# Kernel tuning notes

Measured on AMD Instinct MI355X. Metric: run time of the kernel, lower is better.

Reference implementation:

```python
import jax, jax.numpy as jnp
import numpy as np

N = 65536   # total nodes
E = 1048576 # total edges (avg degree 16)
B = 512     # graphs in batch
H = 4       # gat1 heads
C = 64      # per-head channels / GNN_HIDDEN


def segment_softmax(logits, seg, num_segments):
    # numerically stable softmax over segments (PyG softmax semantics, eps=1e-16)
    m = jax.ops.segment_max(logits, seg, num_segments=num_segments)
    m = jnp.where(jnp.isfinite(m), m, 0.0)
    e = jnp.exp(logits - m[seg])
    s = jax.ops.segment_sum(e, seg, num_segments=num_segments)
    return e / (s[seg] + 1e-16)


def gat_conv(x, edge_index, edge_attr, W, att_src, att_dst, We, att_edge, bias, heads, out_ch, concat):
    # PyG GATConv with edge_dim, add_self_loops=False
    n = x.shape[0]
    h = (x @ W).reshape(n, heads, out_ch)                 # (N,H,C)
    src, dst = edge_index[0], edge_index[1]
    a_s = jnp.sum(h * att_src, axis=-1)                   # (N,H)
    a_d = jnp.sum(h * att_dst, axis=-1)                   # (N,H)
    he = (edge_attr @ We).reshape(-1, heads, out_ch)      # (E,H,C)
    a_e = jnp.sum(he * att_edge, axis=-1)                 # (E,H)
    alpha = jax.nn.leaky_relu(a_s[src] + a_d[dst] + a_e, negative_slope=0.2)
    alpha = segment_softmax(alpha, dst, n)                # softmax over incoming edges per dst
    out = jax.ops.segment_sum(h[src] * alpha[..., None], dst, num_segments=n)  # (N,H,C)
    out = out.reshape(n, heads * out_ch) if concat else out.mean(axis=1)
    return out + bias


def setup_inputs() -> dict:
    key = jax.random.key(0)
    ks = jax.random.split(key, 24)
    s = 0.05
    d = {}
    d["global_feat"] = jax.random.normal(ks[0], (B, 512), jnp.float32)
    d["x"] = jax.random.normal(ks[1], (N, 13), jnp.float32)
    d["roi_feats"] = jax.random.normal(ks[2], (N, 256), jnp.float32)
    d["edge_index"] = jax.random.randint(ks[3], (2, E), 0, N)
    d["edge_attr"] = jax.random.normal(ks[4], (E, 5), jnp.float32)
    d["batch_vec"] = jnp.sort(jax.random.randint(ks[5], (N,), 0, B))
    # roi_proj / scene_proj
    d["roi_W"] = jax.random.normal(ks[6], (256, 64), jnp.float32) * s
    d["roi_b"] = jnp.zeros((64,), jnp.float32)
    d["scene_W"] = jax.random.normal(ks[7], (512, 128), jnp.float32) * s
    d["scene_b"] = jnp.zeros((128,), jnp.float32)
    d["g1_W"] = jax.random.normal(ks[8], (77, H * C), jnp.float32) * s
    d["g1_att_src"] = jax.random.normal(ks[9], (H, C), jnp.float32) * s
    d["g1_att_dst"] = jax.random.normal(ks[10], (H, C), jnp.float32) * s
    d["g1_We"] = jax.random.normal(ks[11], (5, H * C), jnp.float32) * s
    d["g1_att_edge"] = jax.random.normal(ks[12], (H, C), jnp.float32) * s
    d["g1_bias"] = jnp.zeros((H * C,), jnp.float32)
    # gat2: 256 -> 64, 1 head
    d["g2_W"] = jax.random.normal(ks[13], (H * C, C), jnp.float32) * s
    d["g2_att_src"] = jax.random.normal(ks[14], (1, C), jnp.float32) * s
    d["g2_att_dst"] = jax.random.normal(ks[15], (1, C), jnp.float32) * s
    d["g2_We"] = jax.random.normal(ks[16], (5, C), jnp.float32) * s
    d["g2_att_edge"] = jax.random.normal(ks[17], (1, C), jnp.float32) * s
    d["g2_bias"] = jnp.zeros((C,), jnp.float32)
    # attention pooling gate + classifier
    d["gate_W"] = jax.random.normal(ks[18], (C, 1), jnp.float32) * s
    d["gate_b"] = jnp.zeros((1,), jnp.float32)
    d["cls1_W"] = jax.random.normal(ks[19], (128 + C, 64), jnp.float32) * s
    d["cls1_b"] = jnp.zeros((64,), jnp.float32)
    d["cls2_W"] = jax.random.normal(ks[20], (64, 3), jnp.float32) * s
    d["cls2_b"] = jnp.zeros((3,), jnp.float32)
    return d


def reference(global_feat, x, roi_feats, edge_index, edge_attr, batch_vec,
              roi_W, roi_b, scene_W, scene_b,
              g1_W, g1_att_src, g1_att_dst, g1_We, g1_att_edge, g1_bias,
              g2_W, g2_att_src, g2_att_dst, g2_We, g2_att_edge, g2_bias,
              gate_W, gate_b, cls1_W, cls1_b, cls2_W, cls2_b):
    scene = global_feat @ scene_W + scene_b                       # (B,128)
    vis = jax.nn.relu(roi_feats @ roi_W + roi_b)                  # (N,64)
    h = jnp.concatenate([x, vis], axis=-1)                        # (N,77)
    h = jax.nn.relu(gat_conv(h, edge_index, edge_attr, g1_W, g1_att_src, g1_att_dst, g1_We, g1_att_edge, g1_bias, H, C, True))
    h = gat_conv(h, edge_index, edge_attr, g2_W, g2_att_src, g2_att_dst, g2_We, g2_att_edge, g2_bias, 1, C, False)  # (N,64)
    # GlobalAttention pooling
    gate = segment_softmax((h @ gate_W + gate_b)[:, 0], batch_vec, B)
    rel = jax.ops.segment_sum(gate[:, None] * h, batch_vec, num_segments=B)  # (B,64)
    comb = jnp.concatenate([scene, rel], axis=-1)                 # (B,192)
    hid = jax.nn.relu(comb @ cls1_W + cls1_b)                     # dropout off (eval)
    return hid @ cls2_W + cls2_b                                  # (B,3)
```

## Files before the change

### kernel.cpp

```cpp
#include <hip/hip_runtime.h>

#define N_NODES 65536
#define N_EDGES 1048576
#define NB      512

typedef unsigned short u16;
typedef unsigned int   u32;
typedef unsigned long long u64;

typedef __attribute__((ext_vector_type(8))) short bf16x8;
typedef __attribute__((ext_vector_type(4))) float f32x4;

__device__ __forceinline__ float bf2f(u16 u) { return __uint_as_float(((u32)u) << 16); }
__device__ __forceinline__ float lo16(u32 u) { return __uint_as_float(u << 16); }
__device__ __forceinline__ float hi16(u32 u) { return __uint_as_float(u & 0xffff0000u); }
__device__ __forceinline__ u16 f2bf(float f) {
    u32 u = __float_as_uint(f);
    u32 r = (u + 0x7fffu + ((u >> 16) & 1u)) >> 16;
    return (u16)r;
}
__device__ __forceinline__ u32 pk2(float a, float b) {
    return (u32)f2bf(a) | ((u32)f2bf(b) << 16);
}
__device__ __forceinline__ float wsum(float v) {
    for (int o = 32; o; o >>= 1) v += __shfl_xor(v, o, 64);
    return v;
}
__device__ __forceinline__ float wmax(float v) {
    for (int o = 32; o; o >>= 1) v = fmaxf(v, __shfl_xor(v, o, 64));
    return v;
}

__global__ void k_prep(const float* g1We, const float* g1ae, const float* g2We, const float* g2ae,
                       float* M1, float* M2) {
    int t = threadIdx.x;
    if (t < 20) {
        int j = t >> 2, h = t & 3;
        float s = 0.f;
        for (int c = 0; c < 64; c++) s += g1We[j * 256 + h * 64 + c] * g1ae[h * 64 + c];
        M1[t] = s;
    } else if (t < 25) {
        int j = t - 20;
        float s = 0.f;
        for (int c = 0; c < 64; c++) s += g2We[j * 64 + c] * g2ae[c];
        M2[j] = s;
    }
}

__global__ void k_wt1(const float* __restrict__ g1W, u16* __restrict__ Wt) {
    int c = blockIdx.x;
    int k = threadIdx.x;
    float v = 0.f;
    if (k < 77) {
        int ko = (k < 64) ? (13 + k) : (k - 64);
        v = g1W[(size_t)ko * 256 + c];
    }
    Wt[(size_t)c * 96 + k] = f2bf(v);
}

__global__ void k_wtv(const float* __restrict__ W, u16* __restrict__ Wt) {
    int c = blockIdx.x;
    int k = threadIdx.x;
    Wt[(size_t)c * 256 + k] = f2bf(W[(size_t)k * 64 + c]);
}

__global__ __launch_bounds__(256) void k_scene(const float* __restrict__ gf, const float* __restrict__ W,
                                               const float* __restrict__ bias, float* __restrict__ scene) {
    int idx = blockIdx.x * 256 + threadIdx.x;
    int b = idx >> 7, j = idx & 127;
    float acc = 0.f;
    for (int k = 0; k < 512; k++) acc += gf[b * 512 + k] * W[k * 128 + j];
    scene[idx] = acc + bias[j];
}

__global__ __launch_bounds__(256) void k_hist(const int* ei, int* cnt) {
    int e = blockIdx.x * 256 + threadIdx.x;
    atomicAdd(&cnt[ei[N_EDGES + e]], 1);
}

__global__ __launch_bounds__(256) void k_scan_blk(const int* __restrict__ cnt, int* __restrict__ pre,
                                                  int* __restrict__ bsum) {
    __shared__ int sd[256];
    int t = threadIdx.x, b = blockIdx.x;
    int base = b * 1024 + t * 4;
    int4 c = *(const int4*)(cnt + base);
    int s = c.x + c.y + c.z + c.w;
    sd[t] = s;
    __syncthreads();
    for (int off = 1; off < 256; off <<= 1) {
        int v = (t >= off) ? sd[t - off] : 0;
        __syncthreads();
        sd[t] += v;
        __syncthreads();
    }
    int excl = sd[t] - s;
    int4 p;
    p.x = excl;
    p.y = excl + c.x;
    p.z = excl + c.x + c.y;
    p.w = excl + c.x + c.y + c.z;
    *(int4*)(pre + base) = p;
    if (t == 255) bsum[b] = sd[255];
}

__global__ __launch_bounds__(64) void k_scan_top(int* bsum) {
    int t = threadIdx.x;
    int v = bsum[t];
    int inc = v;
    for (int off = 1; off < 64; off <<= 1) {
        int u = __shfl_up(inc, off, 64);
        if (t >= off) inc += u;
    }
    bsum[t] = inc - v;
}

__global__ __launch_bounds__(256) void k_scan_fix(const int* __restrict__ pre, const int* __restrict__ bsum,
                                                  int* __restrict__ row_ptr, int* __restrict__ coarse_cur) {
    int i = blockIdx.x * 256 + threadIdx.x;
    int v = pre[i] + bsum[i >> 10];
    row_ptr[i] = v;
    if ((i & 255) == 0) coarse_cur[i >> 8] = v;
    if (i == 0) row_ptr[N_NODES] = N_EDGES;
}

__global__ __launch_bounds__(256) void k_bucket(const int* __restrict__ ei, int* coarse_cur,
                                                u32* __restrict__ bpack, int* __restrict__ bsrc) {
    __shared__ u32 stageP[4096];
    __shared__ int stageS[4096];
    __shared__ int bcnt[256], bscan[256], boff[256], gbase[256];
    int t = threadIdx.x;
    int e0 = blockIdx.x * 4096;
    bcnt[t] = 0;
    __syncthreads();
    int dreg[16], sreg[16];
    for (int it = 0; it < 16; it++) {
        int e = e0 + it * 256 + t;
        int dd = ei[N_EDGES + e];
        dreg[it] = dd;
        sreg[it] = ei[e];
        atomicAdd(&bcnt[dd >> 8], 1);
    }
    __syncthreads();
    int v = bcnt[t];
    bscan[t] = v;
    __syncthreads();
    for (int off = 1; off < 256; off <<= 1) {
        int u = (t >= off) ? bscan[t - off] : 0;
        __syncthreads();
        bscan[t] += u;
        __syncthreads();
    }
    boff[t] = bscan[t] - v;
    gbase[t] = v ? atomicAdd(&coarse_cur[t], v) : 0;
    __syncthreads();
    for (int it = 0; it < 16; it++) {
        int e = e0 + it * 256 + t;
        int b = dreg[it] >> 8;
        int pos = atomicAdd(&boff[b], 1);
        stageP[pos] = ((u32)e << 12) | (u32)(dreg[it] & 255);
        stageS[pos] = sreg[it];
    }
    __syncthreads();
    for (int idx = t; idx < 4096; idx += 256) {
        int lo = 0, hi = 255;
        while (lo < hi) { int mid = (lo + hi) >> 1; if (bscan[mid] > idx) hi = mid; else lo = mid + 1; }
        int b = lo;
        int g = gbase[b] + (idx - (bscan[b] - bcnt[b]));
        bpack[g] = stageP[idx];
        bsrc[g] = stageS[idx];
    }
}

__global__ __launch_bounds__(256) void k_sortb(const u32* __restrict__ bpack, const int* __restrict__ bsrc,
                                               const int* __restrict__ row_ptr,
                                               int* __restrict__ eord, int* __restrict__ ssrc) {
    __shared__ int cur[256];
    int t = threadIdx.x, b = blockIdx.x;
    int nbase = b * 256;
    cur[t] = row_ptr[nbase + t];
    __syncthreads();
    int beg = row_ptr[nbase];
    int end = row_ptr[nbase + 256];
    for (int i = beg + t; i < end; i += 256) {
        u32 wd = bpack[i];
        int src = bsrc[i];
        int d8 = wd & 255;
        int pos = atomicAdd(&cur[d8], 1);
        eord[pos] = (int)(wd >> 12);
        ssrc[pos] = src;
    }
}

__global__ __launch_bounds__(256) void k_payload(const int* __restrict__ eord, const float* __restrict__ ea,
                                                 const float* __restrict__ M1, const float* __restrict__ M2,
                                                 float* __restrict__ a1es, float* __restrict__ a2es) {
    int pos = blockIdx.x * 256 + threadIdx.x;
    int e = eord[pos];
    float v[5];
    for (int j = 0; j < 5; j++) v[j] = ea[(size_t)e * 5 + j];
    float4 o;
    o.x = v[0]*M1[0]  + v[1]*M1[4]  + v[2]*M1[8]  + v[3]*M1[12] + v[4]*M1[16];
    o.y = v[0]*M1[1]  + v[1]*M1[5]  + v[2]*M1[9]  + v[3]*M1[13] + v[4]*M1[17];
    o.z = v[0]*M1[2]  + v[1]*M1[6]  + v[2]*M1[10] + v[3]*M1[14] + v[4]*M1[18];
    o.w = v[0]*M1[3]  + v[1]*M1[7]  + v[2]*M1[11] + v[3]*M1[15] + v[4]*M1[19];
    *(float4*)(a1es + (size_t)pos * 4) = o;
    a2es[pos] = v[0]*M2[0] + v[1]*M2[1] + v[2]*M2[2] + v[3]*M2[3] + v[4]*M2[4];
}

__global__ __launch_bounds__(256) void k_vis(const float* __restrict__ roi, const u16* __restrict__ Wt,
                                             const float* __restrict__ bias, u16* __restrict__ out) {
    __shared__ u16 At[64][264];
    int t = threadIdx.x;
    int w = t >> 6, l = t & 63, lo = l & 15, hi = l >> 4;
    int n0 = blockIdx.x * 64;
    int r = t >> 2, sub = t & 3;
    const float* rp = roi + (size_t)(n0 + r) * 256 + sub * 4;
    #pragma unroll
    for (int q = 0; q < 16; q++) {
        float4 v = *(const float4*)(rp + q * 16);
        uint2 p;
        p.x = pk2(v.x, v.y);
        p.y = pk2(v.z, v.w);
        *(uint2*)&At[r][q * 16 + sub * 4] = p;
    }
    float bb[4][4];
    #pragma unroll
    for (int cb = 0; cb < 4; cb++)
        #pragma unroll
        for (int rg = 0; rg < 4; rg++) bb[cb][rg] = bias[cb * 16 + hi * 4 + rg];
    __syncthreads();
    f32x4 acc[4];
    #pragma unroll
    for (int cb = 0; cb < 4; cb++) acc[cb] = (f32x4){0.f, 0.f, 0.f, 0.f};
    #pragma unroll
    for (int ks = 0; ks < 8; ks++) {
        bf16x8 af = *(const bf16x8*)(&At[w * 16 + lo][ks * 32 + hi * 8]);
        #pragma unroll
        for (int cb = 0; cb < 4; cb++) {
            bf16x8 wf = *(const bf16x8*)(Wt + (size_t)(cb * 16 + lo) * 256 + ks * 32 + hi * 8);
            acc[cb] = __builtin_amdgcn_mfma_f32_16x16x32_bf16(wf, af, acc[cb], 0, 0, 0);
        }
    }
    int nrow = n0 + w * 16 + lo;
    #pragma unroll
    for (int cb = 0; cb < 4; cb++) {
        uint2 p;
        p.x = pk2(fmaxf(acc[cb][0] + bb[cb][0], 0.f), fmaxf(acc[cb][1] + bb[cb][1], 0.f));
        p.y = pk2(fmaxf(acc[cb][2] + bb[cb][2], 0.f), fmaxf(acc[cb][3] + bb[cb][3], 0.f));
        *(uint2*)(out + (size_t)nrow * 64 + cb * 16 + hi * 4) = p;
    }
}

__global__ __launch_bounds__(256) void k_h1(const float* __restrict__ x, const u16* __restrict__ vis,
                                            const u16* __restrict__ Wt,
                                            const float* __restrict__ as_, const float* __restrict__ ad_,
                                            u16* __restrict__ h1, float* __restrict__ a1s,
                                            float* __restrict__ a1d) {
    __shared__ u16 At[64][104];
    int t = threadIdx.x;
    int w = t >> 6, l = t & 63, lo = l & 15, hi = l >> 4;
    int n0 = blockIdx.x * 64;
    int r = t >> 2, sub = t & 3;
    {
        const uint4* vp = (const uint4*)(vis + (size_t)(n0 + r) * 64 + sub * 16);
        uint4 v0 = vp[0], v1 = vp[1];
        *(uint4*)&At[r][sub * 16] = v0;
        *(uint4*)&At[r][sub * 16 + 8] = v1;
        if (sub == 0) {
            const float* xp = x + (size_t)(n0 + r) * 13;
            #pragma unroll
            for (int j = 0; j < 13; j++) At[r][64 + j] = f2bf(xp[j]);
        } else if (sub == 1) {
            #pragma unroll
            for (int j = 77; j < 96; j++) At[r][j] = 0;
        }
    }
    bf16x8 wf[4][3];
    float asv[4][4], adv[4][4];
    #pragma unroll
    for (int cb = 0; cb < 4; cb++) {
        #pragma unroll
        for (int ks = 0; ks < 3; ks++)
            wf[cb][ks] = *(const bf16x8*)(Wt + (size_t)(w * 64 + cb * 16 + lo) * 96 + ks * 32 + hi * 8);
        #pragma unroll
        for (int rg = 0; rg < 4; rg++) {
            asv[cb][rg] = as_[w * 64 + cb * 16 + hi * 4 + rg];
            adv[cb][rg] = ad_[w * 64 + cb * 16 + hi * 4 + rg];
        }
    }
    __syncthreads();
    #pragma unroll
    for (int nb = 0; nb < 4; nb++) {
        f32x4 acc[4];
        #pragma unroll
        for (int cb = 0; cb < 4; cb++) acc[cb] = (f32x4){0.f, 0.f, 0.f, 0.f};
        #pragma unroll
        for (int ks = 0; ks < 3; ks++) {
            bf16x8 af = *(const bf16x8*)(&At[nb * 16 + lo][ks * 32 + hi * 8]);
            #pragma unroll
            for (int cb = 0; cb < 4; cb++)
                acc[cb] = __builtin_amdgcn_mfma_f32_16x16x32_bf16(wf[cb][ks], af, acc[cb], 0, 0, 0);
        }
        int nrow = n0 + nb * 16 + lo;
        float ps = 0.f, pd = 0.f;
        #pragma unroll
        for (int cb = 0; cb < 4; cb++) {
            uint2 p;
            p.x = pk2(acc[cb][0], acc[cb][1]);
            p.y = pk2(acc[cb][2], acc[cb][3]);
            *(uint2*)(h1 + (size_t)nrow * 256 + w * 64 + cb * 16 + hi * 4) = p;
            ps += acc[cb][0] * asv[cb][0] + acc[cb][1] * asv[cb][1]
                + acc[cb][2] * asv[cb][2] + acc[cb][3] * asv[cb][3];
            pd += acc[cb][0] * adv[cb][0] + acc[cb][1] * adv[cb][1]
                + acc[cb][2] * adv[cb][2] + acc[cb][3] * adv[cb][3];
        }
        ps += __shfl_xor(ps, 16, 64); ps += __shfl_xor(ps, 32, 64);
        pd += __shfl_xor(pd, 16, 64); pd += __shfl_xor(pd, 32, 64);
        if (hi == 0) {
            a1s[nrow * 4 + w] = ps;
            a1d[nrow * 4 + w] = pd;
        }
    }
}

__global__ __launch_bounds__(256) void k_h2(const u16* __restrict__ A, const u16* __restrict__ Wt,
                                            const float* __restrict__ as_, const float* __restrict__ ad_,
                                            u16* __restrict__ out, float* __restrict__ a2s,
                                            float* __restrict__ a2d) {
    int t = threadIdx.x;
    int w = t >> 6, l = t & 63, lo = l & 15, hi = l >> 4;
    int nrow = blockIdx.x * 64 + w * 16 + lo;
    f32x4 acc[4];
    #pragma unroll
    for (int cb = 0; cb < 4; cb++) acc[cb] = (f32x4){0.f, 0.f, 0.f, 0.f};
    const u16* ap = A + (size_t)nrow * 256 + hi * 8;
    #pragma unroll
    for (int ks = 0; ks < 8; ks++) {
        bf16x8 af = *(const bf16x8*)(ap + ks * 32);
        #pragma unroll
        for (int cb = 0; cb < 4; cb++) {
            bf16x8 wf = *(const bf16x8*)(Wt + (size_t)(cb * 16 + lo) * 256 + ks * 32 + hi * 8);
            acc[cb] = __builtin_amdgcn_mfma_f32_16x16x32_bf16(wf, af, acc[cb], 0, 0, 0);
        }
    }
    float ps = 0.f, pd = 0.f;
    #pragma unroll
    for (int cb = 0; cb < 4; cb++) {
        uint2 p;
        p.x = pk2(acc[cb][0], acc[cb][1]);
        p.y = pk2(acc[cb][2], acc[cb][3]);
        *(uint2*)(out + (size_t)nrow * 64 + cb * 16 + hi * 4) = p;
        #pragma unroll
        for (int rg = 0; rg < 4; rg++) {
            float a = acc[cb][rg];
            ps += a * as_[cb * 16 + hi * 4 + rg];
            pd += a * ad_[cb * 16 + hi * 4 + rg];
        }
    }
    ps += __shfl_xor(ps, 16, 64); ps += __shfl_xor(ps, 32, 64);
    pd += __shfl_xor(pd, 16, 64); pd += __shfl_xor(pd, 32, 64);
    if (hi == 0) {
        a2s[nrow] = ps;
        a2d[nrow] = pd;
    }
}

__global__ __launch_bounds__(256) void k_sg1(const int* __restrict__ row_ptr, const int* __restrict__ ssrc,
                                             const float* __restrict__ a1s, const float* __restrict__ a1d,
                                             const float* __restrict__ a1es, const u16* __restrict__ h1,
                                             const float* __restrict__ bias, u16* __restrict__ out1) {
    __shared__ float wl[4][1024];
    int t = threadIdx.x;
    int wv = t >> 6, L = t & 63;
    int n = blockIdx.x * 4 + wv;
    int beg = row_ptr[n], deg = row_ptr[n + 1] - beg;
    int lim = (deg < 256) ? deg : 256;
    {
        int h = L >> 4, j = L & 15;
        float adn = a1d[n * 4 + h];
        float m = -3.0e38f, s = 0.f;
        for (int i = j; i < deg; i += 16) {
            int pos = beg + i;
            float l = a1s[ssrc[pos] * 4 + h] + adn + a1es[(size_t)pos * 4 + h];
            l = (l > 0.f) ? l : 0.2f * l;
            if (i < 256) wl[wv][i * 4 + h] = l;
            if (l > m) { s = s * __expf(m - l) + 1.f; m = l; }
            else       { s += __expf(l - m); }
        }
        for (int o = 1; o < 16; o <<= 1) {
            float mo = __shfl_xor(m, o, 64), so = __shfl_xor(s, o, 64);
            float M = fmaxf(m, mo);
            s = s * __expf(m - M) + so * __expf(mo - M);
            m = M;
        }
        float inv = 1.f / (s + 1e-16f);
        for (int i = j; i < lim; i += 16)
            wl[wv][i * 4 + h] = __expf(wl[wv][i * 4 + h] - m) * inv;
    }
    __syncthreads();
    int halfE = L >> 5;
    int L32 = L & 31;
    int hd = L32 >> 3;
    float acc[8];
    #pragma unroll
    for (int j = 0; j < 8; j++) acc[j] = 0.f;
    int last = beg + deg - 1;
    for (int i = 0; i < deg; i += 8) {
        int iA = i + halfE, iB = i + 2 + halfE, iC = i + 4 + halfE, iD = i + 6 + halfE;
        bool vA = iA < deg, vB = iB < deg, vC = iC < deg, vD = iD < deg;
        int cA = vA ? beg + iA : last, cB = vB ? beg + iB : last;
        int cC = vC ? beg + iC : last, cD = vD ? beg + iD : last;
        int sA = ssrc[cA], sB = ssrc[cB], sC = ssrc[cC], sD = ssrc[cD];
        float wA = vA ? wl[wv][iA * 4 + hd] : 0.f;
        float wB = vB ? wl[wv][iB * 4 + hd] : 0.f;
        float wC = vC ? wl[wv][iC * 4 + hd] : 0.f;
        float wD = vD ? wl[wv][iD * 4 + hd] : 0.f;
        uint4 uA = *((const uint4*)(h1 + (size_t)sA * 256) + L32);
        uint4 uB = *((const uint4*)(h1 + (size_t)sB * 256) + L32);
        uint4 uC = *((const uint4*)(h1 + (size_t)sC * 256) + L32);
        uint4 uD = *((const uint4*)(h1 + (size_t)sD * 256) + L32);
        acc[0] += wA * lo16(uA.x) + wB * lo16(uB.x) + wC * lo16(uC.x) + wD * lo16(uD.x);
        acc[1] += wA * hi16(uA.x) + wB * hi16(uB.x) + wC * hi16(uC.x) + wD * hi16(uD.x);
        acc[2] += wA * lo16(uA.y) + wB * lo16(uB.y) + wC * lo16(uC.y) + wD * lo16(uD.y);
        acc[3] += wA * hi16(uA.y) + wB * hi16(uB.y) + wC * hi16(uC.y) + wD * hi16(uD.y);
        acc[4] += wA * lo16(uA.z) + wB * lo16(uB.z) + wC * lo16(uC.z) + wD * lo16(uD.z);
        acc[5] += wA * hi16(uA.z) + wB * hi16(uB.z) + wC * hi16(uC.z) + wD * hi16(uD.z);
        acc[6] += wA * lo16(uA.w) + wB * lo16(uB.w) + wC * lo16(uC.w) + wD * lo16(uD.w);
        acc[7] += wA * hi16(uA.w) + wB * hi16(uB.w) + wC * hi16(uC.w) + wD * hi16(uD.w);
    }
    #pragma unroll
    for (int j = 0; j < 8; j++) acc[j] += __shfl_xor(acc[j], 32, 64);
    if (halfE == 0) {
        float4 b0 = *(const float4*)(bias + 8 * L32);
        float4 b1 = *(const float4*)(bias + 8 * L32 + 4);
        uint4 pk;
        pk.x = (u32)f2bf(fmaxf(acc[0] + b0.x, 0.f)) | ((u32)f2bf(fmaxf(acc[1] + b0.y, 0.f)) << 16);
        pk.y = (u32)f2bf(fmaxf(acc[2] + b0.z, 0.f)) | ((u32)f2bf(fmaxf(acc[3] + b0.w, 0.f)) << 16);
        pk.z = (u32)f2bf(fmaxf(acc[4] + b1.x, 0.f)) | ((u32)f2bf(fmaxf(acc[5] + b1.y, 0.f)) << 16);
        pk.w = (u32)f2bf(fmaxf(acc[6] + b1.z, 0.f)) | ((u32)f2bf(fmaxf(acc[7] + b1.w, 0.f)) << 16);
        *((uint4*)(out1 + (size_t)n * 256) + L32) = pk;
    }
}

__global__ __launch_bounds__(256) void k_sg2(const int* __restrict__ row_ptr, const int* __restrict__ ssrc,
                                             const float* __restrict__ a2s, const float* __restrict__ a2d,
                                             const float* __restrict__ a2es, const u16* __restrict__ h2b,
                                             const float* __restrict__ bias, float* __restrict__ hfin) {
    __shared__ float wl[4][256];
    int t = threadIdx.x;
    int wv = t >> 6, L = t & 63;
    int n = blockIdx.x * 4 + wv;
    int beg = row_ptr[n], deg = row_ptr[n + 1] - beg;
    int lim = (deg < 256) ? deg : 256;
    {
        float adn = a2d[n];
        float m = -3.0e38f, s = 0.f;
        for (int i = L; i < deg; i += 64) {
            int pos = beg + i;
            float l = a2s[ssrc[pos]] + adn + a2es[pos];
            l = (l > 0.f) ? l : 0.2f * l;
            if (i < 256) wl[wv][i] = l;
            if (l > m) { s = s * __expf(m - l) + 1.f; m = l; }
            else       { s += __expf(l - m); }
        }
        for (int o = 1; o < 64; o <<= 1) {
            float mo = __shfl_xor(m, o, 64), so = __shfl_xor(s, o, 64);
            float M = fmaxf(m, mo);
            s = s * __expf(m - M) + so * __expf(mo - M);
            m = M;
        }
        float inv = 1.f / (s + 1e-16f);
        for (int i = L; i < lim; i += 64)
            wl[wv][i] = __expf(wl[wv][i] - m) * inv;
    }
    __syncthreads();
    int halfE = L >> 5;
    int L32 = L & 31;
    float a0 = 0.f, a1v = 0.f;
    int last = beg + deg - 1;
    const u32* h2u = (const u32*)h2b;
    for (int i = 0; i < deg; i += 8) {
        int iA = i + halfE, iB = i + 2 + halfE, iC = i + 4 + halfE, iD = i + 6 + halfE;
        bool vA = iA < deg, vB = iB < deg, vC = iC < deg, vD = iD < deg;
        int cA = vA ? beg + iA : last, cB = vB ? beg + iB : last;
        int cC = vC ? beg + iC : last, cD = vD ? beg + iD : last;
        int sA = ssrc[cA], sB = ssrc[cB], sC = ssrc[cC], sD = ssrc[cD];
        float wA = vA ? wl[wv][iA] : 0.f;
        float wB = vB ? wl[wv][iB] : 0.f;
        float wC = vC ? wl[wv][iC] : 0.f;
        float wD = vD ? wl[wv][iD] : 0.f;
        u32 uA = h2u[(size_t)sA * 32 + L32];
        u32 uB = h2u[(size_t)sB * 32 + L32];
        u32 uC = h2u[(size_t)sC * 32 + L32];
        u32 uD = h2u[(size_t)sD * 32 + L32];
        a0  += wA * lo16(uA) + wB * lo16(uB) + wC * lo16(uC) + wD * lo16(uD);
        a1v += wA * hi16(uA) + wB * hi16(uB) + wC * hi16(uC) + wD * hi16(uD);
    }
    a0  += __shfl_xor(a0, 32, 64);
    a1v += __shfl_xor(a1v, 32, 64);
    if (halfE == 0) {
        float2 o;
        o.x = a0  + bias[2 * L32];
        o.y = a1v + bias[2 * L32 + 1];
        *(float2*)(hfin + (size_t)n * 64 + 2 * L32) = o;
    }
}

__global__ __launch_bounds__(64) void k_pool(const int* __restrict__ bvec, const float* __restrict__ hf,
                                             const float* gateW, const float* gateb,
                                             const float* __restrict__ scene,
                                             const float* c1W, const float* c1b,
                                             const float* c2W, const float* c2b,
                                             float* __restrict__ outp) {
    int b = blockIdx.x, lane = threadIdx.x;
    __shared__ float gwl[64], se[64], comb[192], hid[64];
    gwl[lane] = gateW[lane];
    __syncthreads();
    int s0, s1;
    { int lo = 0, hi = N_NODES; while (lo < hi) { int mid = (lo + hi) >> 1; if (bvec[mid] < b) lo = mid + 1; else hi = mid; } s0 = lo; }
    { int lo = 0, hi = N_NODES; while (lo < hi) { int mid = (lo + hi) >> 1; if (bvec[mid] < b + 1) lo = mid + 1; else hi = mid; } s1 = lo; }
    float gb = gateb[0];
    float m = -3.0e38f, ssum = 0.f, acc = 0.f;
    for (int cs = s0; cs < s1; cs += 64) {
        int cnt = min(64, s1 - cs);
        float l = -3.0e38f;
        if (lane < cnt) {
            int n = cs + lane;
            float d = 0.f;
            for (int i = 0; i < 64; i++) d += hf[(size_t)n * 64 + i] * gwl[i];
            l = d + gb;
        }
        float cm = wmax(l);
        float newm = fmaxf(m, cm);
        float rsc = __expf(m - newm);
        float e = (lane < cnt) ? __expf(l - newm) : 0.f;
        float es = wsum(e);
        ssum = ssum * rsc + es;
        se[lane] = e;
        __syncthreads();
        float a2 = 0.f;
        for (int i = 0; i < cnt; i++) a2 += se[i] * hf[(size_t)(cs + i) * 64 + lane];
        acc = acc * rsc + a2;
        __syncthreads();
        m = newm;
    }
    float rel = acc / (ssum + 1e-16f);
    comb[lane] = scene[b * 128 + lane];
    comb[64 + lane] = scene[b * 128 + 64 + lane];
    comb[128 + lane] = rel;
    __syncthreads();
    float hj = 0.f;
    for (int k = 0; k < 192; k++) hj += comb[k] * c1W[k * 64 + lane];
    hj += c1b[lane];
    hid[lane] = fmaxf(hj, 0.f);
    __syncthreads();
    if (lane < 3) {
        float o = 0.f;
        for (int k = 0; k < 64; k++) o += hid[k] * c2W[k * 3 + lane];
        o += c2b[lane];
        outp[b * 3 + lane] = o;
    }
}

extern "C" void kernel_launch(void* const* d_in, const int* in_sizes, int n_in,
                              void* d_out, int out_size, void* d_ws, size_t ws_size,
                              hipStream_t stream) {
    (void)in_sizes; (void)n_in; (void)out_size; (void)ws_size;
    const float* gf     = (const float*)d_in[0];
    const float* x      = (const float*)d_in[1];
    const float* roi    = (const float*)d_in[2];
    const int*   ei     = (const int*)d_in[3];
    const float* ea     = (const float*)d_in[4];
    const int*   bvec   = (const int*)d_in[5];
    const float* roiW   = (const float*)d_in[6];
    const float* roib   = (const float*)d_in[7];
    const float* sceneW = (const float*)d_in[8];
    const float* sceneb = (const float*)d_in[9];
    const float* g1W    = (const float*)d_in[10];
    const float* g1as   = (const float*)d_in[11];
    const float* g1ad   = (const float*)d_in[12];
    const float* g1We   = (const float*)d_in[13];
    const float* g1ae   = (const float*)d_in[14];
    const float* g1b    = (const float*)d_in[15];
    const float* g2W    = (const float*)d_in[16];
    const float* g2as   = (const float*)d_in[17];
    const float* g2ad   = (const float*)d_in[18];
    const float* g2We   = (const float*)d_in[19];
    const float* g2ae   = (const float*)d_in[20];
    const float* g2b    = (const float*)d_in[21];
    const float* gateW  = (const float*)d_in[22];
    const float* gateb  = (const float*)d_in[23];
    const float* c1W    = (const float*)d_in[24];
    const float* c1b    = (const float*)d_in[25];
    const float* c2W    = (const float*)d_in[26];
    const float* c2b    = (const float*)d_in[27];

    char* w = (char*)d_ws;
    size_t o = 0;
    auto nxt = [&](size_t bytes) -> char* {
        char* p = w + o;
        o += (bytes + 255) & ~(size_t)255;
        return p;
    };
    float* scene  = (float*)nxt((size_t)NB * 128 * 4);
    float* M1     = (float*)nxt(80);
    float* M2     = (float*)nxt(32);
    u16* g1Wt     = (u16*)nxt((size_t)256 * 96 * 2);
    u16* roiWt    = (u16*)nxt((size_t)64 * 256 * 2);
    u16* g2Wt     = (u16*)nxt((size_t)64 * 256 * 2);
    int* cnt      = (int*)nxt((size_t)N_NODES * 4);
    int* pre      = (int*)nxt((size_t)N_NODES * 4);
    int* bsum     = (int*)nxt(64 * 4);
    int* row_ptr  = (int*)nxt((size_t)(N_NODES + 1) * 4);
    int* coarse   = (int*)nxt(256 * 4);
    u32* bpack    = (u32*)nxt((size_t)N_EDGES * 4);
    int* bsrc     = (int*)nxt((size_t)N_EDGES * 4);
    int* eord     = (int*)nxt((size_t)N_EDGES * 4);
    int* ssrc     = (int*)nxt((size_t)N_EDGES * 4);
    float* a1es   = (float*)nxt((size_t)N_EDGES * 16);
    float* a2es   = (float*)nxt((size_t)N_EDGES * 4);
    u16* visb     = (u16*)nxt((size_t)N_NODES * 64 * 2);
    u16* h1       = (u16*)nxt((size_t)N_NODES * 256 * 2);
    u16* out1     = (u16*)nxt((size_t)N_NODES * 256 * 2);
    u16* h2b      = (u16*)nxt((size_t)N_NODES * 64 * 2);
    float* hfin   = (float*)nxt((size_t)N_NODES * 64 * 4);
    float* a1s    = (float*)nxt((size_t)N_NODES * 16);
    float* a1d    = (float*)nxt((size_t)N_NODES * 16);
    float* a2s    = (float*)nxt((size_t)N_NODES * 4);
    float* a2d    = (float*)nxt((size_t)N_NODES * 4);

    hipMemsetAsync(cnt, 0, (size_t)N_NODES * 4, stream);
    k_prep<<<1, 32, 0, stream>>>(g1We, g1ae, g2We, g2ae, M1, M2);
    k_wt1<<<256, 96, 0, stream>>>(g1W, g1Wt);
    k_wtv<<<64, 256, 0, stream>>>(roiW, roiWt);
    k_wtv<<<64, 256, 0, stream>>>(g2W, g2Wt);
    k_scene<<<(NB * 128) / 256, 256, 0, stream>>>(gf, sceneW, sceneb, scene);
    k_hist<<<N_EDGES / 256, 256, 0, stream>>>(ei, cnt);
    k_scan_blk<<<64, 256, 0, stream>>>(cnt, pre, bsum);
    k_scan_top<<<1, 64, 0, stream>>>(bsum);
    k_scan_fix<<<N_NODES / 256, 256, 0, stream>>>(pre, bsum, row_ptr, coarse);
    k_bucket<<<256, 256, 0, stream>>>(ei, coarse, bpack, bsrc);
    k_sortb<<<256, 256, 0, stream>>>(bpack, bsrc, row_ptr, eord, ssrc);
    k_payload<<<N_EDGES / 256, 256, 0, stream>>>(eord, ea, M1, M2, a1es, a2es);
    k_vis<<<N_NODES / 64, 256, 0, stream>>>(roi, roiWt, roib, visb);
    k_h1<<<N_NODES / 64, 256, 0, stream>>>(x, visb, g1Wt, g1as, g1ad, h1, a1s, a1d);
    k_sg1<<<N_NODES / 4, 256, 0, stream>>>(row_ptr, ssrc, a1s, a1d, a1es, h1, g1b, out1);
    k_h2<<<N_NODES / 64, 256, 0, stream>>>(out1, g2Wt, g2as, g2ad, h2b, a2s, a2d);
    k_sg2<<<N_NODES / 4, 256, 0, stream>>>(row_ptr, ssrc, a2s, a2d, a2es, h2b, g2b, hfin);
    k_pool<<<NB, 64, 0, stream>>>(bvec, hfin, gateW, gateb, scene, c1W, c1b, c2W, c2b, (float*)d_out);
}
```

Baseline: 527.4 us.

## Fuse weight prep kernels, fold edge payload into sort, prefetch gathers in aggregation

Merges the four weight-preparation kernels into one launch and folds the edge-attribute payload computation into the bucket-sort kernel, which removes the eord array and one pass over edges. The bucket kernel now takes 2048 edges per block across twice as many blocks. Both aggregation kernels cache source indices in shared memory during the softmax pass and software-prefetch the next group of neighbor rows. The block-wide barrier is replaced with a compiler fence plus s_waitcnt, which relies on each wave only reading its own shared-memory slice. The payload computation now runs per edge inside the sort loop, with scattered edge_attr reads.

New measurement: 538.4 us. 2.1% more time.

```diff
diff --git a/kernel.cpp b/kernel.cpp
--- a/kernel.cpp
+++ b/kernel.cpp
@@ -31,37 +31,44 @@
     return v;
 }
 
-__global__ void k_prep(const float* g1We, const float* g1ae, const float* g2We, const float* g2ae,
-                       float* M1, float* M2) {
-    int t = threadIdx.x;
-    if (t < 20) {
-        int j = t >> 2, h = t & 3;
-        float s = 0.f;
-        for (int c = 0; c < 64; c++) s += g1We[j * 256 + h * 64 + c] * g1ae[h * 64 + c];
-        M1[t] = s;
-    } else if (t < 25) {
-        int j = t - 20;
-        float s = 0.f;
-        for (int c = 0; c < 64; c++) s += g2We[j * 64 + c] * g2ae[c];
-        M2[j] = s;
-    }
-}
-
-__global__ void k_wt1(const float* __restrict__ g1W, u16* __restrict__ Wt) {
-    int c = blockIdx.x;
-    int k = threadIdx.x;
-    float v = 0.f;
-    if (k < 77) {
-        int ko = (k < 64) ? (13 + k) : (k - 64);
-        v = g1W[(size_t)ko * 256 + c];
-    }
-    Wt[(size_t)c * 96 + k] = f2bf(v);
-}
-
-__global__ void k_wtv(const float* __restrict__ W, u16* __restrict__ Wt) {
-    int c = blockIdx.x;
-    int k = threadIdx.x;
-    Wt[(size_t)c * 256 + k] = f2bf(W[(size_t)k * 64 + c]);
+__global__ __launch_bounds__(512) void k_wprep(const float* __restrict__ g1W, const float* __restrict__ roiW,
+                                               const float* __restrict__ g2W,
+                                               const float* __restrict__ g1We, const float* __restrict__ g1ae,
+                                               const float* __restrict__ g2We, const float* __restrict__ g2ae,
+                                               u16* __restrict__ g1Wt, u16* __restrict__ roiWt,
+                                               u16* __restrict__ g2Wt, float* __restrict__ M1,
+                                               float* __restrict__ M2) {
+    int b = blockIdx.x, t = threadIdx.x;
+    if (b < 48) {
+        int idx = b * 512 + t;
+        int c = idx / 96, k = idx - 96 * c;
+        float v = 0.f;
+        if (k < 77) {
+            int ko = (k < 64) ? (13 + k) : (k - 64);
+            v = g1W[(size_t)ko * 256 + c];
+        }
+        g1Wt[idx] = f2bf(v);
+    } else if (b < 80) {
+        int idx = (b - 48) * 512 + t;
+        int c = idx >> 8, k = idx & 255;
+        roiWt[idx] = f2bf(roiW[(size_t)k * 64 + c]);
+    } else if (b < 112) {
+        int idx = (b - 80) * 512 + t;
+        int c = idx >> 8, k = idx & 255;
+        g2Wt[idx] = f2bf(g2W[(size_t)k * 64 + c]);
+    } else {
+        if (t < 20) {
+            int j = t >> 2, h = t & 3;
+            float s = 0.f;
+            for (int c = 0; c < 64; c++) s += g1We[j * 256 + h * 64 + c] * g1ae[h * 64 + c];
+            M1[t] = s;
+        } else if (t < 25) {
+            int j = t - 20;
+            float s = 0.f;
+            for (int c = 0; c < 64; c++) s += g2We[j * 64 + c] * g2ae[c];
+            M2[j] = s;
+        }
+    }
 }
 
 __global__ __launch_bounds__(256) void k_scene(const float* __restrict__ gf, const float* __restrict__ W,
@@ -125,15 +132,15 @@
 
 __global__ __launch_bounds__(256) void k_bucket(const int* __restrict__ ei, int* coarse_cur,
                                                 u32* __restrict__ bpack, int* __restrict__ bsrc) {
-    __shared__ u32 stageP[4096];
-    __shared__ int stageS[4096];
+    __shared__ u32 stageP[2048];
+    __shared__ int stageS[2048];
     __shared__ int bcnt[256], bscan[256], boff[256], gbase[256];
     int t = threadIdx.x;
-    int e0 = blockIdx.x * 4096;
+    int e0 = blockIdx.x * 2048;
     bcnt[t] = 0;
     __syncthreads();
-    int dreg[16], sreg[16];
-    for (int it = 0; it < 16; it++) {
+    int dreg[8], sreg[8];
+    for (int it = 0; it < 8; it++) {
         int e = e0 + it * 256 + t;
         int dd = ei[N_EDGES + e];
         dreg[it] = dd;
@@ -153,7 +160,7 @@
     boff[t] = bscan[t] - v;
     gbase[t] = v ? atomicAdd(&coarse_cur[t], v) : 0;
     __syncthreads();
-    for (int it = 0; it < 16; it++) {
+    for (int it = 0; it < 8; it++) {
         int e = e0 + it * 256 + t;
         int b = dreg[it] >> 8;
         int pos = atomicAdd(&boff[b], 1);
@@ -161,7 +168,7 @@
         stageS[pos] = sreg[it];
     }
     __syncthreads();
-    for (int idx = t; idx < 4096; idx += 256) {
+    for (int idx = t; idx < 2048; idx += 256) {
         int lo = 0, hi = 255;
         while (lo < hi) { int mid = (lo + hi) >> 1; if (bscan[mid] > idx) hi = mid; else lo = mid + 1; }
         int b = lo;
@@ -171,40 +178,40 @@
     }
 }
 
-__global__ __launch_bounds__(256) void k_sortb(const u32* __restrict__ bpack, const int* __restrict__ bsrc,
-                                               const int* __restrict__ row_ptr,
-                                               int* __restrict__ eord, int* __restrict__ ssrc) {
+__global__ __launch_bounds__(256) void k_sortp(const u32* __restrict__ bpack, const int* __restrict__ bsrc,
+                                               const int* __restrict__ row_ptr, const float* __restrict__ ea,
+                                               const float* __restrict__ M1, const float* __restrict__ M2,
+                                               int* __restrict__ ssrc, float* __restrict__ a1es,
+                                               float* __restrict__ a2es) {
     __shared__ int cur[256];
     int t = threadIdx.x, b = blockIdx.x;
     int nbase = b * 256;
     cur[t] = row_ptr[nbase + t];
     __syncthreads();
+    float m1[20], m2[5];
+    #pragma unroll
+    for (int j = 0; j < 20; j++) m1[j] = M1[j];
+    #pragma unroll
+    for (int j = 0; j < 5; j++) m2[j] = M2[j];
     int beg = row_ptr[nbase];
     int end = row_ptr[nbase + 256];
     for (int i = beg + t; i < end; i += 256) {
         u32 wd = bpack[i];
         int src = bsrc[i];
         int d8 = wd & 255;
+        int e = (int)(wd >> 12);
         int pos = atomicAdd(&cur[d8], 1);
-        eord[pos] = (int)(wd >> 12);
         ssrc[pos] = src;
-    }
-}
-
-__global__ __launch_bounds__(256) void k_payload(const int* __restrict__ eord, const float* __restrict__ ea,
-                                                 const float* __restrict__ M1, const float* __restrict__ M2,
-                                                 float* __restrict__ a1es, float* __restrict__ a2es) {
-    int pos = blockIdx.x * 256 + threadIdx.x;
-    int e = eord[pos];
-    float v[5];
-    for (int j = 0; j < 5; j++) v[j] = ea[(size_t)e * 5 + j];
-    float4 o;
-    o.x = v[0]*M1[0]  + v[1]*M1[4]  + v[2]*M1[8]  + v[3]*M1[12] + v[4]*M1[16];
-    o.y = v[0]*M1[1]  + v[1]*M1[5]  + v[2]*M1[9]  + v[3]*M1[13] + v[4]*M1[17];
-    o.z = v[0]*M1[2]  + v[1]*M1[6]  + v[2]*M1[10] + v[3]*M1[14] + v[4]*M1[18];
-    o.w = v[0]*M1[3]  + v[1]*M1[7]  + v[2]*M1[11] + v[3]*M1[15] + v[4]*M1[19];
-    *(float4*)(a1es + (size_t)pos * 4) = o;
-    a2es[pos] = v[0]*M2[0] + v[1]*M2[1] + v[2]*M2[2] + v[3]*M2[3] + v[4]*M2[4];
+        const float* ep = ea + (size_t)e * 5;
+        float v0 = ep[0], v1 = ep[1], v2 = ep[2], v3 = ep[3], v4 = ep[4];
+        float4 o;
+        o.x = v0*m1[0]  + v1*m1[4]  + v2*m1[8]  + v3*m1[12] + v4*m1[16];
+        o.y = v0*m1[1]  + v1*m1[5]  + v2*m1[9]  + v3*m1[13] + v4*m1[17];
+        o.z = v0*m1[2]  + v1*m1[6]  + v2*m1[10] + v3*m1[14] + v4*m1[18];
+        o.w = v0*m1[3]  + v1*m1[7]  + v2*m1[11] + v3*m1[15] + v4*m1[19];
+        *(float4*)(a1es + (size_t)pos * 4) = o;
+        a2es[pos] = v0*m2[0] + v1*m2[1] + v2*m2[2] + v3*m2[3] + v4*m2[4];
+    }
 }
 
 __global__ __launch_bounds__(256) void k_vis(const float* __restrict__ roi, const u16* __restrict__ Wt,
@@ -323,53 +330,12 @@
     }
 }
 
-__global__ __launch_bounds__(256) void k_h2(const u16* __restrict__ A, const u16* __restrict__ Wt,
-                                            const float* __restrict__ as_, const float* __restrict__ ad_,
-                                            u16* __restrict__ out, float* __restrict__ a2s,
-                                            float* __restrict__ a2d) {
-    int t = threadIdx.x;
-    int w = t >> 6, l = t & 63, lo = l & 15, hi = l >> 4;
-    int nrow = blockIdx.x * 64 + w * 16 + lo;
-    f32x4 acc[4];
-    #pragma unroll
-    for (int cb = 0; cb < 4; cb++) acc[cb] = (f32x4){0.f, 0.f, 0.f, 0.f};
-    const u16* ap = A + (size_t)nrow * 256 + hi * 8;
-    #pragma unroll
-    for (int ks = 0; ks < 8; ks++) {
-        bf16x8 af = *(const bf16x8*)(ap + ks * 32);
-        #pragma unroll
-        for (int cb = 0; cb < 4; cb++) {
-            bf16x8 wf = *(const bf16x8*)(Wt + (size_t)(cb * 16 + lo) * 256 + ks * 32 + hi * 8);
-            acc[cb] = __builtin_amdgcn_mfma_f32_16x16x32_bf16(wf, af, acc[cb], 0, 0, 0);
-        }
-    }
-    float ps = 0.f, pd = 0.f;
-    #pragma unroll
-    for (int cb = 0; cb < 4; cb++) {
-        uint2 p;
-        p.x = pk2(acc[cb][0], acc[cb][1]);
-        p.y = pk2(acc[cb][2], acc[cb][3]);
-        *(uint2*)(out + (size_t)nrow * 64 + cb * 16 + hi * 4) = p;
-        #pragma unroll
-        for (int rg = 0; rg < 4; rg++) {
-            float a = acc[cb][rg];
-            ps += a * as_[cb * 16 + hi * 4 + rg];
-            pd += a * ad_[cb * 16 + hi * 4 + rg];
-        }
-    }
-    ps += __shfl_xor(ps, 16, 64); ps += __shfl_xor(ps, 32, 64);
-    pd += __shfl_xor(pd, 16, 64); pd += __shfl_xor(pd, 32, 64);
-    if (hi == 0) {
-        a2s[nrow] = ps;
-        a2d[nrow] = pd;
-    }
-}
-
 __global__ __launch_bounds__(256) void k_sg1(const int* __restrict__ row_ptr, const int* __restrict__ ssrc,
                                              const float* __restrict__ a1s, const float* __restrict__ a1d,
                                              const float* __restrict__ a1es, const u16* __restrict__ h1,
                                              const float* __restrict__ bias, u16* __restrict__ out1) {
     __shared__ float wl[4][1024];
+    __shared__ int   sl[4][256];
     int t = threadIdx.x;
     int wv = t >> 6, L = t & 63;
     int n = blockIdx.x * 4 + wv;
@@ -381,7 +347,9 @@
         float m = -3.0e38f, s = 0.f;
         for (int i = j; i < deg; i += 16) {
             int pos = beg + i;
-            float l = a1s[ssrc[pos] * 4 + h] + adn + a1es[(size_t)pos * 4 + h];
+            int sv = ssrc[pos];
+            if (h == 0 && i < 256) sl[wv][i] = sv;
+            float l = a1s[sv * 4 + h] + adn + a1es[(size_t)pos * 4 + h];
             l = (l > 0.f) ? l : 0.2f * l;
             if (i < 256) wl[wv][i * 4 + h] = l;
             if (l > m) { s = s * __expf(m - l) + 1.f; m = l; }
@@ -397,36 +365,44 @@
         for (int i = j; i < lim; i += 16)
             wl[wv][i * 4 + h] = __expf(wl[wv][i * 4 + h] - m) * inv;
     }
-    __syncthreads();
+    asm volatile("" ::: "memory");
+    __builtin_amdgcn_s_waitcnt(0);
     int halfE = L >> 5;
     int L32 = L & 31;
     int hd = L32 >> 3;
     float acc[8];
     #pragma unroll
     for (int j = 0; j < 8; j++) acc[j] = 0.f;
-    int last = beg + deg - 1;
+    uint4 U[4];
+    float W[4];
+    #pragma unroll
+    for (int k = 0; k < 4; k++) {
+        int ii = 2 * k + halfE;
+        bool v = ii < deg;
+        int s = v ? sl[wv][ii] : 0;
+        W[k] = v ? wl[wv][ii * 4 + hd] : 0.f;
+        U[k] = *((const uint4*)(h1 + (size_t)s * 256) + L32);
+    }
     for (int i = 0; i < deg; i += 8) {
-        int iA = i + halfE, iB = i + 2 + halfE, iC = i + 4 + halfE, iD = i + 6 + halfE;
-        bool vA = iA < deg, vB = iB < deg, vC = iC < deg, vD = iD < deg;
-        int cA = vA ? beg + iA : last, cB = vB ? beg + iB : last;
-        int cC = vC ? beg + iC : last, cD = vD ? beg + iD : last;
-        int sA = ssrc[cA], sB = ssrc[cB], sC = ssrc[cC], sD = ssrc[cD];
-        float wA = vA ? wl[wv][iA * 4 + hd] : 0.f;
-        float wB = vB ? wl[wv][iB * 4 + hd] : 0.f;
-        float wC = vC ? wl[wv][iC * 4 + hd] : 0.f;
-        float wD = vD ? wl[wv][iD * 4 + hd] : 0.f;
-        uint4 uA = *((const uint4*)(h1 + (size_t)sA * 256) + L32);
-        uint4 uB = *((const uint4*)(h1 + (size_t)sB * 256) + L32);
-        uint4 uC = *((const uint4*)(h1 + (size_t)sC * 256) + L32);
-        uint4 uD = *((const uint4*)(h1 + (size_t)sD * 256) + L32);
-        acc[0] += wA * lo16(uA.x) + wB * lo16(uB.x) + wC * lo16(uC.x) + wD * lo16(uD.x);
-        acc[1] += wA * hi16(uA.x) + wB * hi16(uB.x) + wC * hi16(uC.x) + wD * hi16(uD.x);
-        acc[2] += wA * lo16(uA.y) + wB * lo16(uB.y) + wC * lo16(uC.y) + wD * lo16(uD.y);
-        acc[3] += wA * hi16(uA.y) + wB * hi16(uB.y) + wC * hi16(uC.y) + wD * hi16(uD.y);
-        acc[4] += wA * lo16(uA.z) + wB * lo16(uB.z) + wC * lo16(uC.z) + wD * lo16(uD.z);
-        acc[5] += wA * hi16(uA.z) + wB * hi16(uB.z) + wC * hi16(uC.z) + wD * hi16(uD.z);
-        acc[6] += wA * lo16(uA.w) + wB * lo16(uB.w) + wC * lo16(uC.w) + wD * lo16(uD.w);
-        acc[7] += wA * hi16(uA.w) + wB * hi16(uB.w) + wC * hi16(uC.w) + wD * hi16(uD.w);
+        uint4 C0 = U[0], C1 = U[1], C2 = U[2], C3 = U[3];
+        float W0 = W[0], W1 = W[1], W2 = W[2], W3 = W[3];
+        int ib = i + 8;
+        #pragma unroll
+        for (int k = 0; k < 4; k++) {
+            int ii = ib + 2 * k + halfE;
+            bool v = ii < deg;
+            int s = v ? sl[wv][ii] : 0;
+            W[k] = v ? wl[wv][ii * 4 + hd] : 0.f;
+            U[k] = *((const uint4*)(h1 + (size_t)s * 256) + L32);
+        }
+        acc[0] += W0 * lo16(C0.x) + W1 * lo16(C1.x) + W2 * lo16(C2.x) + W3 * lo16(C3.x);
+        acc[1] += W0 * hi16(C0.x) + W1 * hi16(C1.x) + W2 * hi16(C2.x) + W3 * hi16(C3.x);
+        acc[2] += W0 * lo16(C0.y) + W1 * lo16(C1.y) + W2 * lo16(C2.y) + W3 * lo16(C3.y);
+        acc[3] += W0 * hi16(C0.y) + W1 * hi16(C1.y) + W2 * hi16(C2.y) + W3 * hi16(C3.y);
+        acc[4] += W0 * lo16(C0.z) + W1 * lo16(C1.z) + W2 * lo16(C2.z) + W3 * lo16(C3.z);
+        acc[5] += W0 * hi16(C0.z) + W1 * hi16(C1.z) + W2 * hi16(C2.z) + W3 * hi16(C3.z);
+        acc[6] += W0 * lo16(C0.w) + W1 * lo16(C1.w) + W2 * lo16(C2.w) + W3 * lo16(C3.w);
+        acc[7] += W0 * hi16(C0.w) + W1 * hi16(C1.w) + W2 * hi16(C2.w) + W3 * hi16(C3.w);
     }
     #pragma unroll
     for (int j = 0; j < 8; j++) acc[j] += __shfl_xor(acc[j], 32, 64);
@@ -442,11 +418,54 @@
     }
 }
 
+__global__ __launch_bounds__(256) void k_h2(const u16* __restrict__ A, const u16* __restrict__ Wt,
+                                            const float* __restrict__ as_, const float* __restrict__ ad_,
+                                            u16* __restrict__ out, float* __restrict__ a2s,
+                                            float* __restrict__ a2d) {
+    int t = threadIdx.x;
+    int w = t >> 6, l = t & 63, lo = l & 15, hi = l >> 4;
+    int nrow = blockIdx.x * 64 + w * 16 + lo;
+    f32x4 acc[4];
+    #pragma unroll
+    for (int cb = 0; cb < 4; cb++) acc[cb] = (f32x4){0.f, 0.f, 0.f, 0.f};
+    const u16* ap = A + (size_t)nrow * 256 + hi * 8;
+    #pragma unroll
+    for (int ks = 0; ks < 8; ks++) {
+        bf16x8 af = *(const bf16x8*)(ap + ks * 32);
+        #pragma unroll
+        for (int cb = 0; cb < 4; cb++) {
+            bf16x8 wf = *(const bf16x8*)(Wt + (size_t)(cb * 16 + lo) * 256 + ks * 32 + hi * 8);
+            acc[cb] = __builtin_amdgcn_mfma_f32_16x16x32_bf16(wf, af, acc[cb], 0, 0, 0);
+        }
+    }
+    float ps = 0.f, pd = 0.f;
+    #pragma unroll
+    for (int cb = 0; cb < 4; cb++) {
+        uint2 p;
+        p.x = pk2(acc[cb][0], acc[cb][1]);
+        p.y = pk2(acc[cb][2], acc[cb][3]);
+        *(uint2*)(out + (size_t)nrow * 64 + cb * 16 + hi * 4) = p;
+        #pragma unroll
+        for (int rg = 0; rg < 4; rg++) {
+            float a = acc[cb][rg];
+            ps += a * as_[cb * 16 + hi * 4 + rg];
+            pd += a * ad_[cb * 16 + hi * 4 + rg];
+        }
+    }
+    ps += __shfl_xor(ps, 16, 64); ps += __shfl_xor(ps, 32, 64);
+    pd += __shfl_xor(pd, 16, 64); pd += __shfl_xor(pd, 32, 64);
+    if (hi == 0) {
+        a2s[nrow] = ps;
+        a2d[nrow] = pd;
+    }
+}
+
 __global__ __launch_bounds__(256) void k_sg2(const int* __restrict__ row_ptr, const int* __restrict__ ssrc,
                                              const float* __restrict__ a2s, const float* __restrict__ a2d,
                                              const float* __restrict__ a2es, const u16* __restrict__ h2b,
                                              const float* __restrict__ bias, float* __restrict__ hfin) {
     __shared__ float wl[4][256];
+    __shared__ int   sl[4][256];
     int t = threadIdx.x;
     int wv = t >> 6, L = t & 63;
     int n = blockIdx.x * 4 + wv;
@@ -457,7 +476,9 @@
         float m = -3.0e38f, s = 0.f;
         for (int i = L; i < deg; i += 64) {
             int pos = beg + i;
-            float l = a2s[ssrc[pos]] + adn + a2es[pos];
+            int sv = ssrc[pos];
+            if (i < 256) sl[wv][i] = sv;
+            float l = a2s[sv] + adn + a2es[pos];
             l = (l > 0.f) ? l : 0.2f * l;
             if (i < 256) wl[wv][i] = l;
             if (l > m) { s = s * __expf(m - l) + 1.f; m = l; }
@@ -473,28 +494,36 @@
         for (int i = L; i < lim; i += 64)
             wl[wv][i] = __expf(wl[wv][i] - m) * inv;
     }
-    __syncthreads();
+    asm volatile("" ::: "memory");
+    __builtin_amdgcn_s_waitcnt(0);
     int halfE = L >> 5;
     int L32 = L & 31;
     float a0 = 0.f, a1v = 0.f;
-    int last = beg + deg - 1;
     const u32* h2u = (const u32*)h2b;
+    u32 U[4];
+    float W[4];
+    #pragma unroll
+    for (int k = 0; k < 4; k++) {
+        int ii = 2 * k + halfE;
+        bool v = ii < deg;
+        int s = v ? sl[wv][ii] : 0;
+        W[k] = v ? wl[wv][ii] : 0.f;
+        U[k] = h2u[(size_t)s * 32 + L32];
+    }
     for (int i = 0; i < deg; i += 8) {
-        int iA = i + halfE, iB = i + 2 + halfE, iC = i + 4 + halfE, iD = i + 6 + halfE;
-        bool vA = iA < deg, vB = iB < deg, vC = iC < deg, vD = iD < deg;
-        int cA = vA ? beg + iA : last, cB = vB ? beg + iB : last;
-        int cC = vC ? beg + iC : last, cD = vD ? beg + iD : last;
-        int sA = ssrc[cA], sB = ssrc[cB], sC = ssrc[cC], sD = ssrc[cD];
-        float wA = vA ? wl[wv][iA] : 0.f;
-        float wB = vB ? wl[wv][iB] : 0.f;
-        float wC = vC ? wl[wv][iC] : 0.f;
-        float wD = vD ? wl[wv][iD] : 0.f;
-        u32 uA = h2u[(size_t)sA * 32 + L32];
-        u32 uB = h2u[(size_t)sB * 32 + L32];
-        u32 uC = h2u[(size_t)sC * 32 + L32];
-        u32 uD = h2u[(size_t)sD * 32 + L32];
-        a0  += wA * lo16(uA) + wB * lo16(uB) + wC * lo16(uC) + wD * lo16(uD);
-        a1v += wA * hi16(uA) + wB * hi16(uB) + wC * hi16(uC) + wD * hi16(uD);
+        u32 C0 = U[0], C1 = U[1], C2 = U[2], C3 = U[3];
+        float W0 = W[0], W1 = W[1], W2 = W[2], W3 = W[3];
+        int ib = i + 8;
+        #pragma unroll
+        for (int k = 0; k < 4; k++) {
+            int ii = ib + 2 * k + halfE;
+            bool v = ii < deg;
+            int s = v ? sl[wv][ii] : 0;
+            W[k] = v ? wl[wv][ii] : 0.f;
+            U[k] = h2u[(size_t)s * 32 + L32];
+        }
+        a0  += W0 * lo16(C0) + W1 * lo16(C1) + W2 * lo16(C2) + W3 * lo16(C3);
+        a1v += W0 * hi16(C0) + W1 * hi16(C1) + W2 * hi16(C2) + W3 * hi16(C3);
     }
     a0  += __shfl_xor(a0, 32, 64);
     a1v += __shfl_xor(a1v, 32, 64);
@@ -615,7 +644,6 @@
     int* coarse   = (int*)nxt(256 * 4);
     u32* bpack    = (u32*)nxt((size_t)N_EDGES * 4);
     int* bsrc     = (int*)nxt((size_t)N_EDGES * 4);
-    int* eord     = (int*)nxt((size_t)N_EDGES * 4);
     int* ssrc     = (int*)nxt((size_t)N_EDGES * 4);
     float* a1es   = (float*)nxt((size_t)N_EDGES * 16);
     float* a2es   = (float*)nxt((size_t)N_EDGES * 4);
@@ -630,18 +658,15 @@
     float* a2d    = (float*)nxt((size_t)N_NODES * 4);
 
     hipMemsetAsync(cnt, 0, (size_t)N_NODES * 4, stream);
-    k_prep<<<1, 32, 0, stream>>>(g1We, g1ae, g2We, g2ae, M1, M2);
-    k_wt1<<<256, 96, 0, stream>>>(g1W, g1Wt);
-    k_wtv<<<64, 256, 0, stream>>>(roiW, roiWt);
-    k_wtv<<<64, 256, 0, stream>>>(g2W, g2Wt);
+    k_wprep<<<113, 512, 0, stream>>>(g1W, roiW, g2W, g1We, g1ae, g2We, g2ae,
+                                     g1Wt, roiWt, g2Wt, M1, M2);
     k_scene<<<(NB * 128) / 256, 256, 0, stream>>>(gf, sceneW, sceneb, scene);
     k_hist<<<N_EDGES / 256, 256, 0, stream>>>(ei, cnt);
     k_scan_blk<<<64, 256, 0, stream>>>(cnt, pre, bsum);
     k_scan_top<<<1, 64, 0, stream>>>(bsum);
     k_scan_fix<<<N_NODES / 256, 256, 0, stream>>>(pre, bsum, row_ptr, coarse);
-    k_bucket<<<256, 256, 0, stream>>>(ei, coarse, bpack, bsrc);
-    k_sortb<<<256, 256, 0, stream>>>(bpack, bsrc, row_ptr, eord, ssrc);
-    k_payload<<<N_EDGES / 256, 256, 0, stream>>>(eord, ea, M1, M2, a1es, a2es);
+    k_bucket<<<512, 256, 0, stream>>>(ei, coarse, bpack, bsrc);
+    k_sortp<<<256, 256, 0, stream>>>(bpack, bsrc, row_ptr, ea, M1, M2, ssrc, a1es, a2es);
     k_vis<<<N_NODES / 64, 256, 0, stream>>>(roi, roiWt, roib, visb);
     k_h1<<<N_NODES / 64, 256, 0, stream>>>(x, visb, g1Wt, g1as, g1ad, h1, a1s, a1d);
     k_sg1<<<N_NODES / 4, 256, 0, stream>>>(row_ptr, ssrc, a1s, a1d, a1es, h1, g1b, out1);
```
